# Optimization experiments

Hardware: AMD Instinct MI355X
Metric: run time of the kernel (lower is better)

Reference implementation:

```python
import jax, jax.numpy as jnp
import numpy as np

B, S, D = 4, 2048, 1024  # batch, seq (== context_size), d_in == d_out


def setup_inputs() -> dict:
    key = jax.random.key(0)
    ks = jax.random.split(key, 4)
    scale = 1.0 / np.sqrt(D)
    return {
        "x": jax.random.normal(ks[0], (B, S, D), dtype=jnp.float32),
        "Wq": jax.random.normal(ks[1], (D, D), dtype=jnp.float32) * scale,
        "bq": jnp.zeros((D,), dtype=jnp.float32),
        "Wk": jax.random.normal(ks[2], (D, D), dtype=jnp.float32) * scale,
        "bk": jnp.zeros((D,), dtype=jnp.float32),
        "Wv": jax.random.normal(ks[3], (D, D), dtype=jnp.float32) * scale,
        "bv": jnp.zeros((D,), dtype=jnp.float32),
    }


def reference(x, Wq, bq, Wk, bk, Wv, bv):
    # x: [B, S, D]. Linear layers: y = x @ W^T + b (torch convention: W is [out, in];
    # here W is stored [in, out] already so y = x @ W + b).
    q = jnp.einsum("bsd,df->bsf", x, Wq) + bq
    k = jnp.einsum("bsd,df->bsf", x, Wk) + bk
    v = jnp.einsum("bsd,df->bsf", x, Wv) + bv
    scores = jnp.einsum("bqf,bkf->bqk", q, k)  # [B, S, S]
    causal = jnp.tril(jnp.ones((S, S), dtype=bool))  # mask upper triangle (future)
    scores = jnp.where(causal, scores, -jnp.inf)
    # original divides by sqrt(d_out) after masking
    attn = jax.nn.softmax(scores * (1.0 / jnp.sqrt(jnp.asarray(D, scores.dtype))), axis=-1)
    # dropout rate = 0.0 (identity)
    return jnp.einsum("bqk,bkf->bqf", attn, v)
```

## Files before the change

### kernel.cpp

```cpp
#include <hip/hip_runtime.h>
#include <cstdint>
#include <cstddef>


typedef __attribute__((ext_vector_type(8))) __bf16 bf16x8;
typedef __attribute__((ext_vector_type(4))) float f32x4;
typedef __attribute__((ext_vector_type(4))) float float4v;
typedef __attribute__((ext_vector_type(8))) unsigned short u16x8;
typedef __attribute__((ext_vector_type(4))) unsigned short u16x4;

#define DEVI static __device__ __forceinline__

static constexpr int BB = 4;
static constexpr int SS = 2048;
static constexpr int DD = 1024;
static constexpr float SCALE = 0.03125f;

DEVI unsigned short f2bf(float f) {
  unsigned int u = __builtin_bit_cast(unsigned int, f);
  u += 0x7fffu + ((u >> 16) & 1u);
  return (unsigned short)(u >> 16);
}
DEVI float bf2f(unsigned short h) {
  unsigned int u = ((unsigned int)h) << 16;
  return __builtin_bit_cast(float, u);
}

DEVI void gload16(const void* g, void* l) {
  __builtin_amdgcn_global_load_lds(
      (const __attribute__((address_space(1))) unsigned int*)g,
      (__attribute__((address_space(3))) unsigned int*)l, 16, 0, 0);
}

DEVI void gemm_core(const unsigned short* __restrict__ A,
                    const unsigned short* __restrict__ Bt,
                    int lda, int ldb, int m0, int n0, int K,
                    unsigned short* As, unsigned short* Bs,
                    f32x4 acc[4][4]) {
  const int t = threadIdx.x;
  const int l = t & 63, w = t >> 6;
  const int wr = w >> 1, wc = w & 1;
  const int srow = t >> 2;
  const int scol = (t & 3) * 8;
  const unsigned short* ga0 = A + (size_t)(m0 + srow) * lda + scol;
  const unsigned short* ga1 = ga0 + (size_t)64 * lda;
  const unsigned short* gb0 = Bt + (size_t)(n0 + srow) * ldb + scol;
  const unsigned short* gb1 = gb0 + (size_t)64 * ldb;
  unsigned short* la0 = As + t * 8;
  unsigned short* la1 = As + 2048 + t * 8;
  unsigned short* lb0 = Bs + t * 8;
  unsigned short* lb1 = Bs + 2048 + t * 8;
  const int aoff = (wr * 64 + (l & 15)) * 32 + (l >> 4) * 8;
  const int boff = (wc * 64 + (l & 15)) * 32 + (l >> 4) * 8;
  for (int kk = 0; kk < K; kk += 32) {
    gload16(ga0 + kk, la0);
    gload16(ga1 + kk, la1);
    gload16(gb0 + kk, lb0);
    gload16(gb1 + kk, lb1);
    __syncthreads();
    bf16x8 av[4], bv[4];
#pragma unroll
    for (int i = 0; i < 4; ++i) av[i] = *(const bf16x8*)(As + aoff + i * 512);
#pragma unroll
    for (int i = 0; i < 4; ++i) bv[i] = *(const bf16x8*)(Bs + boff + i * 512);
#pragma unroll
    for (int mi = 0; mi < 4; ++mi)
#pragma unroll
      for (int ni = 0; ni < 4; ++ni)
        acc[mi][ni] = __builtin_amdgcn_mfma_f32_16x16x32_bf16(
            av[mi], bv[ni], acc[mi][ni], 0, 0, 0);
    __syncthreads();
  }
}

__global__ __launch_bounds__(256) void k_conv_x(const float* __restrict__ x,
                                                unsigned short* __restrict__ xb) {
  size_t i = ((size_t)blockIdx.x * 256 + threadIdx.x) * 4;
  float4v v = *(const float4v*)(x + i);
  u16x4 o;
#pragma unroll
  for (int j = 0; j < 4; ++j) o[j] = f2bf(v[j]);
  *(u16x4*)(xb + i) = o;
}

__global__ __launch_bounds__(256) void k_prep_w(const float* __restrict__ Wq,
                                                const float* __restrict__ Wk,
                                                const float* __restrict__ Wv,
                                                unsigned short* __restrict__ Wt) {
  const int z = blockIdx.z;
  const float* W = (z == 0) ? Wq : (z == 1) ? Wk : Wv;
  unsigned short* O = Wt + (size_t)z * DD * DD;
  const int c0 = blockIdx.x * 64, r0 = blockIdx.y * 64;
  __shared__ unsigned short T[64][72];
  const int t = threadIdx.x;
#pragma unroll
  for (int i = 0; i < 4; ++i) {
    int idx = t + i * 256;
    int row = idx >> 4;
    int c4 = (idx & 15) * 4;
    float4v v = *(const float4v*)(W + (size_t)(r0 + row) * DD + c0 + c4);
#pragma unroll
    for (int j = 0; j < 4; ++j) T[row][c4 + j] = f2bf(v[j]);
  }
  __syncthreads();
#pragma unroll
  for (int i = 0; i < 2; ++i) {
    int idx = t + i * 256;
    int n = idx >> 3;
    int g = (idx & 7) * 8;
    u16x8 u;
#pragma unroll
    for (int j = 0; j < 8; ++j) u[j] = T[g + j][n];
    *(u16x8*)(O + (size_t)(c0 + n) * DD + r0 + g) = u;
  }
}

__global__ __launch_bounds__(256) void k_qk_gemm(
    const unsigned short* __restrict__ xb,
    const unsigned short* __restrict__ Wqt,
    const unsigned short* __restrict__ Wkt,
    const float* __restrict__ bq, const float* __restrict__ bk,
    unsigned short* __restrict__ qb, unsigned short* __restrict__ kb) {
  __shared__ unsigned short As[4096], Bs[4096];
  const int z = blockIdx.z;
  const unsigned short* Bt = z ? Wkt : Wqt;
  const float* bias = z ? bk : bq;
  unsigned short* C = z ? kb : qb;
  const int m0 = blockIdx.x * 128, n0 = blockIdx.y * 128;
  f32x4 acc[4][4];
#pragma unroll
  for (int i = 0; i < 4; ++i)
#pragma unroll
    for (int j = 0; j < 4; ++j) acc[i][j] = f32x4{0.f, 0.f, 0.f, 0.f};
  gemm_core(xb, Bt, DD, DD, m0, n0, DD, As, Bs, acc);
  const int t = threadIdx.x, l = t & 63, w = t >> 6, wr = w >> 1, wc = w & 1;
  const int fr = (l >> 4) * 4, fc = l & 15;
#pragma unroll
  for (int mi = 0; mi < 4; ++mi)
#pragma unroll
    for (int ni = 0; ni < 4; ++ni) {
      int gc = n0 + wc * 64 + ni * 16 + fc;
      float bv_ = bias[gc];
#pragma unroll
      for (int r = 0; r < 4; ++r) {
        int gr = m0 + wr * 64 + mi * 16 + fr + r;
        C[(size_t)gr * DD + gc] = f2bf(acc[mi][ni][r] + bv_);
      }
    }
}

__global__ __launch_bounds__(256) void k_vt_gemm(
    const unsigned short* __restrict__ Wvt,
    const unsigned short* __restrict__ xb,
    const float* __restrict__ bv, unsigned short* __restrict__ vt) {
  __shared__ unsigned short As[4096], Bs[4096];
  const int b = blockIdx.z;
  const int m0 = blockIdx.x * 128;
  const int n0 = blockIdx.y * 128;
  f32x4 acc[4][4];
#pragma unroll
  for (int i = 0; i < 4; ++i)
#pragma unroll
    for (int j = 0; j < 4; ++j) acc[i][j] = f32x4{0.f, 0.f, 0.f, 0.f};
  gemm_core(Wvt, xb + (size_t)b * SS * DD, DD, DD, m0, n0, DD, As, Bs, acc);
  unsigned short* C = vt + (size_t)b * DD * SS;
  const int t = threadIdx.x, l = t & 63, w = t >> 6, wr = w >> 1, wc = w & 1;
  const int fr = (l >> 4) * 4, fc = l & 15;
#pragma unroll
  for (int mi = 0; mi < 4; ++mi)
#pragma unroll
    for (int ni = 0; ni < 4; ++ni) {
      int gc = n0 + wc * 64 + ni * 16 + fc;
#pragma unroll
      for (int r = 0; r < 4; ++r) {
        int gr = m0 + wr * 64 + mi * 16 + fr + r;
        C[(size_t)gr * SS + gc] = f2bf(acc[mi][ni][r] + bv[gr]);
      }
    }
}

__global__ __launch_bounds__(256) void k_scores(
    const unsigned short* __restrict__ qb,
    const unsigned short* __restrict__ kb,
    unsigned short* __restrict__ P,
    float* __restrict__ mT, float* __restrict__ lT) {
  const int kt = blockIdx.x, qt = blockIdx.y, b = blockIdx.z;
  if (kt > qt) return;
  __shared__ unsigned short As[4096], Bs[4096];
  __shared__ float redm[2][128];
  __shared__ float redl[2][128];
  f32x4 acc[4][4];
#pragma unroll
  for (int i = 0; i < 4; ++i)
#pragma unroll
    for (int j = 0; j < 4; ++j) acc[i][j] = f32x4{0.f, 0.f, 0.f, 0.f};
  const unsigned short* qp = qb + (size_t)b * SS * DD;
  const unsigned short* kp = kb + (size_t)b * SS * DD;
  gemm_core(qp, kp, DD, DD, qt * 128, kt * 128, DD, As, Bs, acc);

  const int t = threadIdx.x, l = t & 63, w = t >> 6, wr = w >> 1, wc = w & 1;
  const int fr = (l >> 4) * 4, fc = l & 15;
  const bool diag = (kt == qt);
#pragma unroll
  for (int mi = 0; mi < 4; ++mi)
#pragma unroll
    for (int ni = 0; ni < 4; ++ni) {
      int lc = wc * 64 + ni * 16 + fc;
#pragma unroll
      for (int r = 0; r < 4; ++r) {
        int lr = wr * 64 + mi * 16 + fr + r;
        float s = acc[mi][ni][r] * SCALE;
        if (diag && lc > lr) s = -INFINITY;
        acc[mi][ni][r] = s;
      }
    }
  float rmax[4][4];
#pragma unroll
  for (int mi = 0; mi < 4; ++mi)
#pragma unroll
    for (int r = 0; r < 4; ++r) {
      float m = acc[mi][0][r];
#pragma unroll
      for (int ni = 1; ni < 4; ++ni) m = fmaxf(m, acc[mi][ni][r]);
      rmax[mi][r] = m;
    }
#pragma unroll
  for (int d = 1; d < 16; d <<= 1)
#pragma unroll
    for (int mi = 0; mi < 4; ++mi)
#pragma unroll
      for (int r = 0; r < 4; ++r)
        rmax[mi][r] = fmaxf(rmax[mi][r], __shfl_xor(rmax[mi][r], d));
  if ((l & 15) == 0) {
#pragma unroll
    for (int mi = 0; mi < 4; ++mi)
#pragma unroll
      for (int r = 0; r < 4; ++r)
        redm[wc][wr * 64 + mi * 16 + fr + r] = rmax[mi][r];
  }
  __syncthreads();
  float mtv[4][4];
#pragma unroll
  for (int mi = 0; mi < 4; ++mi)
#pragma unroll
    for (int r = 0; r < 4; ++r) {
      int row_l = wr * 64 + mi * 16 + fr + r;
      mtv[mi][r] = fmaxf(redm[0][row_l], redm[1][row_l]);
    }
  float rsum[4][4];
#pragma unroll
  for (int mi = 0; mi < 4; ++mi)
#pragma unroll
    for (int r = 0; r < 4; ++r) rsum[mi][r] = 0.f;
#pragma unroll
  for (int mi = 0; mi < 4; ++mi)
#pragma unroll
    for (int ni = 0; ni < 4; ++ni)
#pragma unroll
      for (int r = 0; r < 4; ++r) {
        float p = __expf(acc[mi][ni][r] - mtv[mi][r]);
        acc[mi][ni][r] = p;
        rsum[mi][r] += p;
      }
#pragma unroll
  for (int d = 1; d < 16; d <<= 1)
#pragma unroll
    for (int mi = 0; mi < 4; ++mi)
#pragma unroll
      for (int r = 0; r < 4; ++r)
        rsum[mi][r] += __shfl_xor(rsum[mi][r], d);
  if ((l & 15) == 0) {
#pragma unroll
    for (int mi = 0; mi < 4; ++mi)
#pragma unroll
      for (int r = 0; r < 4; ++r)
        redl[wc][wr * 64 + mi * 16 + fr + r] = rsum[mi][r];
  }
  __syncthreads();
  if (wc == 0 && (l & 15) == 0) {
#pragma unroll
    for (int mi = 0; mi < 4; ++mi)
#pragma unroll
      for (int r = 0; r < 4; ++r) {
        int row_l = wr * 64 + mi * 16 + fr + r;
        int gq = qt * 128 + row_l;
        mT[((size_t)b * 16 + kt) * SS + gq] = mtv[mi][r];
        lT[((size_t)b * 16 + kt) * SS + gq] = redl[0][row_l] + redl[1][row_l];
      }
  }
  unsigned short* Pp = P + (size_t)b * SS * SS;
#pragma unroll
  for (int mi = 0; mi < 4; ++mi)
#pragma unroll
    for (int ni = 0; ni < 4; ++ni) {
      int gc = kt * 128 + wc * 64 + ni * 16 + fc;
#pragma unroll
      for (int r = 0; r < 4; ++r) {
        int gr = qt * 128 + wr * 64 + mi * 16 + fr + r;
        Pp[(size_t)gr * SS + gc] = f2bf(acc[mi][ni][r]);
      }
    }
}

__global__ __launch_bounds__(256) void k_combine(float* __restrict__ mT,
                                                 const float* __restrict__ lT) {
  const int idx = blockIdx.x * 256 + threadIdx.x;
  const int b = idx >> 11, q = idx & 2047;
  const int qt = q >> 7;
  float mv[16];
  float m = -INFINITY;
#pragma unroll
  for (int kt = 0; kt < 16; ++kt)
    if (kt <= qt) {
      mv[kt] = mT[((size_t)b * 16 + kt) * SS + q];
      m = fmaxf(m, mv[kt]);
    }
  float lsum = 0.f;
#pragma unroll
  for (int kt = 0; kt < 16; ++kt)
    if (kt <= qt) lsum += lT[((size_t)b * 16 + kt) * SS + q] * __expf(mv[kt] - m);
  const float inv = 1.f / lsum;
#pragma unroll
  for (int kt = 0; kt < 16; ++kt)
    if (kt <= qt) mT[((size_t)b * 16 + kt) * SS + q] = __expf(mv[kt] - m) * inv;
}

__global__ __launch_bounds__(256) void k_fixup(unsigned short* __restrict__ P,
                                               const float* __restrict__ F) {
  const int q = blockIdx.x, b = blockIdx.y, t = threadIdx.x;
  const int qt = q >> 7, kt = t >> 4;
  if (kt > qt) return;
  const float f = F[((size_t)b * 16 + kt) * SS + q];
  unsigned short* p = P + (size_t)b * SS * SS + (size_t)q * SS + t * 8;
  u16x8 v = *(const u16x8*)p;
#pragma unroll
  for (int j = 0; j < 8; ++j) v[j] = f2bf(bf2f(v[j]) * f);
  *(u16x8*)p = v;
}

__global__ __launch_bounds__(256) void k_pv(const unsigned short* __restrict__ P,
                                            const unsigned short* __restrict__ vt,
                                            float* __restrict__ out) {
  __shared__ unsigned short As[4096], Bs[4096];
  const int b = blockIdx.z;
  const int n0 = blockIdx.x * 128;
  const int qt = blockIdx.y;
  const int m0 = qt * 128;
  const int Kmax = (qt + 1) * 128;
  f32x4 acc[4][4];
#pragma unroll
  for (int i = 0; i < 4; ++i)
#pragma unroll
    for (int j = 0; j < 4; ++j) acc[i][j] = f32x4{0.f, 0.f, 0.f, 0.f};
  gemm_core(P + (size_t)b * SS * SS, vt + (size_t)b * DD * SS, SS, SS,
            m0, n0, Kmax, As, Bs, acc);
  float* O = out + (size_t)b * SS * DD;
  const int t = threadIdx.x, l = t & 63, w = t >> 6, wr = w >> 1, wc = w & 1;
  const int fr = (l >> 4) * 4, fc = l & 15;
#pragma unroll
  for (int mi = 0; mi < 4; ++mi)
#pragma unroll
    for (int ni = 0; ni < 4; ++ni) {
      int gc = n0 + wc * 64 + ni * 16 + fc;
#pragma unroll
      for (int r = 0; r < 4; ++r) {
        int gr = m0 + wr * 64 + mi * 16 + fr + r;
        O[(size_t)gr * DD + gc] = acc[mi][ni][r];
      }
    }
}

extern "C" void kernel_launch(void* const* d_in, const int* in_sizes, int n_in,
                              void* d_out, int out_size, void* d_ws, size_t ws_size,
                              hipStream_t stream) {
  (void)in_sizes; (void)n_in; (void)out_size; (void)ws_size;
  const float* x  = (const float*)d_in[0];
  const float* Wq = (const float*)d_in[1];
  const float* bq = (const float*)d_in[2];
  const float* Wk = (const float*)d_in[3];
  const float* bk = (const float*)d_in[4];
  const float* Wv = (const float*)d_in[5];
  const float* bv = (const float*)d_in[6];
  float* out = (float*)d_out;

  char* w = (char*)d_ws;
  unsigned short* xb  = (unsigned short*)(w + 0);
  unsigned short* Wt  = (unsigned short*)(w + 16777216);
  unsigned short* qb  = (unsigned short*)(w + 23068672);
  unsigned short* kb  = (unsigned short*)(w + 39845888);
  unsigned short* vt  = (unsigned short*)(w + 56623104);
  unsigned short* P   = (unsigned short*)(w + 73400320);
  float*          mT  = (float*)(w + 106954752);
  float*          lT  = (float*)(w + 107479040);
  unsigned short* Wqt = Wt;
  unsigned short* Wkt = Wt + (size_t)DD * DD;
  unsigned short* Wvt = Wt + (size_t)2 * DD * DD;

  k_conv_x<<<dim3(8192), dim3(256), 0, stream>>>(x, xb);
  k_prep_w<<<dim3(16, 16, 3), dim3(256), 0, stream>>>(Wq, Wk, Wv, Wt);
  k_qk_gemm<<<dim3(64, 8, 2), dim3(256), 0, stream>>>(xb, Wqt, Wkt, bq, bk, qb, kb);
  k_vt_gemm<<<dim3(8, 16, 4), dim3(256), 0, stream>>>(Wvt, xb, bv, vt);
  k_scores<<<dim3(16, 16, 4), dim3(256), 0, stream>>>(qb, kb, P, mT, lT);
  k_combine<<<dim3(32), dim3(256), 0, stream>>>(mT, lT);
  k_fixup<<<dim3(2048, 4), dim3(256), 0, stream>>>(P, mT);
  k_pv<<<dim3(8, 16, 4), dim3(256), 0, stream>>>(P, vt, out);
}
```

Measured before the change: 305.4 us.

## Fold softmax rescale into PV GEMM and use 512-thread GEMM blocks

Removes the separate fixup pass that rescaled every P tile in global memory. The PV kernel now accumulates each 128-wide key chunk into a temporary accumulator and scales it by the per-row, per-chunk factor before adding it to the output. All GEMM kernels also switch from 256-thread blocks with 4x4 MFMA tiles per wave to 512-thread blocks with 4x2 tiles per wave, which lowers register use per wave and adds more waves. The cost is extra per-chunk scaling arithmetic in PV and more LDS traffic per MFMA, since each wave now reuses less data.

```diff
diff --git a/kernel.cpp b/kernel.cpp
--- a/kernel.cpp
+++ b/kernel.cpp
@@ -11,7 +11,6 @@
 
 #define DEVI static __device__ __forceinline__
 
-static constexpr int BB = 4;
 static constexpr int SS = 2048;
 static constexpr int DD = 1024;
 static constexpr float SCALE = 0.03125f;
@@ -32,41 +31,35 @@
       (__attribute__((address_space(3))) unsigned int*)l, 16, 0, 0);
 }
 
-DEVI void gemm_core(const unsigned short* __restrict__ A,
-                    const unsigned short* __restrict__ Bt,
-                    int lda, int ldb, int m0, int n0, int K,
-                    unsigned short* As, unsigned short* Bs,
-                    f32x4 acc[4][4]) {
+DEVI void gemm_core512(const unsigned short* __restrict__ A,
+                       const unsigned short* __restrict__ Bt,
+                       int lda, int ldb, int m0, int n0, int K,
+                       unsigned short* As, unsigned short* Bs,
+                       f32x4 acc[4][2]) {
   const int t = threadIdx.x;
   const int l = t & 63, w = t >> 6;
-  const int wr = w >> 1, wc = w & 1;
+  const int wr = w >> 2, wc = w & 3;
   const int srow = t >> 2;
   const int scol = (t & 3) * 8;
-  const unsigned short* ga0 = A + (size_t)(m0 + srow) * lda + scol;
-  const unsigned short* ga1 = ga0 + (size_t)64 * lda;
-  const unsigned short* gb0 = Bt + (size_t)(n0 + srow) * ldb + scol;
-  const unsigned short* gb1 = gb0 + (size_t)64 * ldb;
-  unsigned short* la0 = As + t * 8;
-  unsigned short* la1 = As + 2048 + t * 8;
-  unsigned short* lb0 = Bs + t * 8;
-  unsigned short* lb1 = Bs + 2048 + t * 8;
+  const unsigned short* ga = A + (size_t)(m0 + srow) * lda + scol;
+  const unsigned short* gb = Bt + (size_t)(n0 + srow) * ldb + scol;
+  unsigned short* la = As + t * 8;
+  unsigned short* lb = Bs + t * 8;
   const int aoff = (wr * 64 + (l & 15)) * 32 + (l >> 4) * 8;
-  const int boff = (wc * 64 + (l & 15)) * 32 + (l >> 4) * 8;
+  const int boff = (wc * 32 + (l & 15)) * 32 + (l >> 4) * 8;
   for (int kk = 0; kk < K; kk += 32) {
-    gload16(ga0 + kk, la0);
-    gload16(ga1 + kk, la1);
-    gload16(gb0 + kk, lb0);
-    gload16(gb1 + kk, lb1);
+    gload16(ga + kk, la);
+    gload16(gb + kk, lb);
     __syncthreads();
-    bf16x8 av[4], bv[4];
+    bf16x8 av[4], bv[2];
 #pragma unroll
     for (int i = 0; i < 4; ++i) av[i] = *(const bf16x8*)(As + aoff + i * 512);
 #pragma unroll
-    for (int i = 0; i < 4; ++i) bv[i] = *(const bf16x8*)(Bs + boff + i * 512);
-#pragma unroll
-    for (int mi = 0; mi < 4; ++mi)
-#pragma unroll
-      for (int ni = 0; ni < 4; ++ni)
+    for (int i = 0; i < 2; ++i) bv[i] = *(const bf16x8*)(Bs + boff + i * 512);
+#pragma unroll
+    for (int mi = 0; mi < 4; ++mi)
+#pragma unroll
+      for (int ni = 0; ni < 2; ++ni)
         acc[mi][ni] = __builtin_amdgcn_mfma_f32_16x16x32_bf16(
             av[mi], bv[ni], acc[mi][ni], 0, 0, 0);
     __syncthreads();
@@ -115,7 +108,7 @@
   }
 }
 
-__global__ __launch_bounds__(256) void k_qk_gemm(
+__global__ __launch_bounds__(512, 4) void k_qk_gemm(
     const unsigned short* __restrict__ xb,
     const unsigned short* __restrict__ Wqt,
     const unsigned short* __restrict__ Wkt,
@@ -127,19 +120,19 @@
   const float* bias = z ? bk : bq;
   unsigned short* C = z ? kb : qb;
   const int m0 = blockIdx.x * 128, n0 = blockIdx.y * 128;
-  f32x4 acc[4][4];
+  f32x4 acc[4][2];
 #pragma unroll
   for (int i = 0; i < 4; ++i)
 #pragma unroll
-    for (int j = 0; j < 4; ++j) acc[i][j] = f32x4{0.f, 0.f, 0.f, 0.f};
-  gemm_core(xb, Bt, DD, DD, m0, n0, DD, As, Bs, acc);
-  const int t = threadIdx.x, l = t & 63, w = t >> 6, wr = w >> 1, wc = w & 1;
+    for (int j = 0; j < 2; ++j) acc[i][j] = f32x4{0.f, 0.f, 0.f, 0.f};
+  gemm_core512(xb, Bt, DD, DD, m0, n0, DD, As, Bs, acc);
+  const int t = threadIdx.x, l = t & 63, w = t >> 6, wr = w >> 2, wc = w & 3;
   const int fr = (l >> 4) * 4, fc = l & 15;
 #pragma unroll
   for (int mi = 0; mi < 4; ++mi)
 #pragma unroll
-    for (int ni = 0; ni < 4; ++ni) {
-      int gc = n0 + wc * 64 + ni * 16 + fc;
+    for (int ni = 0; ni < 2; ++ni) {
+      int gc = n0 + wc * 32 + ni * 16 + fc;
       float bv_ = bias[gc];
 #pragma unroll
       for (int r = 0; r < 4; ++r) {
@@ -149,7 +142,7 @@
     }
 }
 
-__global__ __launch_bounds__(256) void k_vt_gemm(
+__global__ __launch_bounds__(512, 4) void k_vt_gemm(
     const unsigned short* __restrict__ Wvt,
     const unsigned short* __restrict__ xb,
     const float* __restrict__ bv, unsigned short* __restrict__ vt) {
@@ -157,20 +150,20 @@
   const int b = blockIdx.z;
   const int m0 = blockIdx.x * 128;
   const int n0 = blockIdx.y * 128;
-  f32x4 acc[4][4];
+  f32x4 acc[4][2];
 #pragma unroll
   for (int i = 0; i < 4; ++i)
 #pragma unroll
-    for (int j = 0; j < 4; ++j) acc[i][j] = f32x4{0.f, 0.f, 0.f, 0.f};
-  gemm_core(Wvt, xb + (size_t)b * SS * DD, DD, DD, m0, n0, DD, As, Bs, acc);
+    for (int j = 0; j < 2; ++j) acc[i][j] = f32x4{0.f, 0.f, 0.f, 0.f};
+  gemm_core512(Wvt, xb + (size_t)b * SS * DD, DD, DD, m0, n0, DD, As, Bs, acc);
   unsigned short* C = vt + (size_t)b * DD * SS;
-  const int t = threadIdx.x, l = t & 63, w = t >> 6, wr = w >> 1, wc = w & 1;
+  const int t = threadIdx.x, l = t & 63, w = t >> 6, wr = w >> 2, wc = w & 3;
   const int fr = (l >> 4) * 4, fc = l & 15;
 #pragma unroll
   for (int mi = 0; mi < 4; ++mi)
 #pragma unroll
-    for (int ni = 0; ni < 4; ++ni) {
-      int gc = n0 + wc * 64 + ni * 16 + fc;
+    for (int ni = 0; ni < 2; ++ni) {
+      int gc = n0 + wc * 32 + ni * 16 + fc;
 #pragma unroll
       for (int r = 0; r < 4; ++r) {
         int gr = m0 + wr * 64 + mi * 16 + fr + r;
@@ -179,7 +172,7 @@
     }
 }
 
-__global__ __launch_bounds__(256) void k_scores(
+__global__ __launch_bounds__(512, 4) void k_scores(
     const unsigned short* __restrict__ qb,
     const unsigned short* __restrict__ kb,
     unsigned short* __restrict__ P,
@@ -187,25 +180,25 @@
   const int kt = blockIdx.x, qt = blockIdx.y, b = blockIdx.z;
   if (kt > qt) return;
   __shared__ unsigned short As[4096], Bs[4096];
-  __shared__ float redm[2][128];
-  __shared__ float redl[2][128];
-  f32x4 acc[4][4];
+  __shared__ float redm[4][128];
+  __shared__ float redl[4][128];
+  f32x4 acc[4][2];
 #pragma unroll
   for (int i = 0; i < 4; ++i)
 #pragma unroll
-    for (int j = 0; j < 4; ++j) acc[i][j] = f32x4{0.f, 0.f, 0.f, 0.f};
+    for (int j = 0; j < 2; ++j) acc[i][j] = f32x4{0.f, 0.f, 0.f, 0.f};
   const unsigned short* qp = qb + (size_t)b * SS * DD;
   const unsigned short* kp = kb + (size_t)b * SS * DD;
-  gemm_core(qp, kp, DD, DD, qt * 128, kt * 128, DD, As, Bs, acc);
-
-  const int t = threadIdx.x, l = t & 63, w = t >> 6, wr = w >> 1, wc = w & 1;
+  gemm_core512(qp, kp, DD, DD, qt * 128, kt * 128, DD, As, Bs, acc);
+
+  const int t = threadIdx.x, l = t & 63, w = t >> 6, wr = w >> 2, wc = w & 3;
   const int fr = (l >> 4) * 4, fc = l & 15;
   const bool diag = (kt == qt);
 #pragma unroll
   for (int mi = 0; mi < 4; ++mi)
 #pragma unroll
-    for (int ni = 0; ni < 4; ++ni) {
-      int lc = wc * 64 + ni * 16 + fc;
+    for (int ni = 0; ni < 2; ++ni) {
+      int lc = wc * 32 + ni * 16 + fc;
 #pragma unroll
       for (int r = 0; r < 4; ++r) {
         int lr = wr * 64 + mi * 16 + fr + r;
@@ -218,12 +211,8 @@
 #pragma unroll
   for (int mi = 0; mi < 4; ++mi)
 #pragma unroll
-    for (int r = 0; r < 4; ++r) {
-      float m = acc[mi][0][r];
-#pragma unroll
-      for (int ni = 1; ni < 4; ++ni) m = fmaxf(m, acc[mi][ni][r]);
-      rmax[mi][r] = m;
-    }
+    for (int r = 0; r < 4; ++r)
+      rmax[mi][r] = fmaxf(acc[mi][0][r], acc[mi][1][r]);
 #pragma unroll
   for (int d = 1; d < 16; d <<= 1)
 #pragma unroll
@@ -245,22 +234,19 @@
 #pragma unroll
     for (int r = 0; r < 4; ++r) {
       int row_l = wr * 64 + mi * 16 + fr + r;
-      mtv[mi][r] = fmaxf(redm[0][row_l], redm[1][row_l]);
+      mtv[mi][r] = fmaxf(fmaxf(redm[0][row_l], redm[1][row_l]),
+                         fmaxf(redm[2][row_l], redm[3][row_l]));
     }
   float rsum[4][4];
 #pragma unroll
   for (int mi = 0; mi < 4; ++mi)
 #pragma unroll
-    for (int r = 0; r < 4; ++r) rsum[mi][r] = 0.f;
-#pragma unroll
-  for (int mi = 0; mi < 4; ++mi)
-#pragma unroll
-    for (int ni = 0; ni < 4; ++ni)
+    for (int ni = 0; ni < 2; ++ni)
 #pragma unroll
       for (int r = 0; r < 4; ++r) {
         float p = __expf(acc[mi][ni][r] - mtv[mi][r]);
         acc[mi][ni][r] = p;
-        rsum[mi][r] += p;
+        if (ni == 0) rsum[mi][r] = p; else rsum[mi][r] += p;
       }
 #pragma unroll
   for (int d = 1; d < 16; d <<= 1)
@@ -285,15 +271,16 @@
         int row_l = wr * 64 + mi * 16 + fr + r;
         int gq = qt * 128 + row_l;
         mT[((size_t)b * 16 + kt) * SS + gq] = mtv[mi][r];
-        lT[((size_t)b * 16 + kt) * SS + gq] = redl[0][row_l] + redl[1][row_l];
+        lT[((size_t)b * 16 + kt) * SS + gq] =
+            redl[0][row_l] + redl[1][row_l] + redl[2][row_l] + redl[3][row_l];
       }
   }
   unsigned short* Pp = P + (size_t)b * SS * SS;
 #pragma unroll
   for (int mi = 0; mi < 4; ++mi)
 #pragma unroll
-    for (int ni = 0; ni < 4; ++ni) {
-      int gc = kt * 128 + wc * 64 + ni * 16 + fc;
+    for (int ni = 0; ni < 2; ++ni) {
+      int gc = kt * 128 + wc * 32 + ni * 16 + fc;
 #pragma unroll
       for (int r = 0; r < 4; ++r) {
         int gr = qt * 128 + wr * 64 + mi * 16 + fr + r;
@@ -325,47 +312,80 @@
     if (kt <= qt) mT[((size_t)b * 16 + kt) * SS + q] = __expf(mv[kt] - m) * inv;
 }
 
-__global__ __launch_bounds__(256) void k_fixup(unsigned short* __restrict__ P,
-                                               const float* __restrict__ F) {
-  const int q = blockIdx.x, b = blockIdx.y, t = threadIdx.x;
-  const int qt = q >> 7, kt = t >> 4;
-  if (kt > qt) return;
-  const float f = F[((size_t)b * 16 + kt) * SS + q];
-  unsigned short* p = P + (size_t)b * SS * SS + (size_t)q * SS + t * 8;
-  u16x8 v = *(const u16x8*)p;
-#pragma unroll
-  for (int j = 0; j < 8; ++j) v[j] = f2bf(bf2f(v[j]) * f);
-  *(u16x8*)p = v;
-}
-
-__global__ __launch_bounds__(256) void k_pv(const unsigned short* __restrict__ P,
-                                            const unsigned short* __restrict__ vt,
-                                            float* __restrict__ out) {
+__global__ __launch_bounds__(512, 4) void k_pv(
+    const unsigned short* __restrict__ P,
+    const unsigned short* __restrict__ vt,
+    const float* __restrict__ F, float* __restrict__ out) {
   __shared__ unsigned short As[4096], Bs[4096];
+  __shared__ float Flds[2048];
   const int b = blockIdx.z;
   const int n0 = blockIdx.x * 128;
   const int qt = blockIdx.y;
   const int m0 = qt * 128;
-  const int Kmax = (qt + 1) * 128;
-  f32x4 acc[4][4];
+  const int nchunk = qt + 1;
+  const int t = threadIdx.x, l = t & 63, w = t >> 6, wr = w >> 2, wc = w & 3;
+  const int fr = (l >> 4) * 4, fc = l & 15;
+  for (int idx = t; idx < nchunk * 128; idx += 512)
+    Flds[idx] = F[((size_t)b * 16 + (idx >> 7)) * SS + m0 + (idx & 127)];
+  f32x4 accO[4][2], accP[4][2];
 #pragma unroll
   for (int i = 0; i < 4; ++i)
 #pragma unroll
-    for (int j = 0; j < 4; ++j) acc[i][j] = f32x4{0.f, 0.f, 0.f, 0.f};
-  gemm_core(P + (size_t)b * SS * SS, vt + (size_t)b * DD * SS, SS, SS,
-            m0, n0, Kmax, As, Bs, acc);
+    for (int j = 0; j < 2; ++j) {
+      accO[i][j] = f32x4{0.f, 0.f, 0.f, 0.f};
+      accP[i][j] = f32x4{0.f, 0.f, 0.f, 0.f};
+    }
+  const unsigned short* Pp = P + (size_t)b * SS * SS;
+  const unsigned short* Vp = vt + (size_t)b * DD * SS;
+  const int srow = t >> 2, scol = (t & 3) * 8;
+  const unsigned short* ga = Pp + (size_t)(m0 + srow) * SS + scol;
+  const unsigned short* gb = Vp + (size_t)(n0 + srow) * SS + scol;
+  unsigned short* la = As + t * 8;
+  unsigned short* lb = Bs + t * 8;
+  const int aoff = (wr * 64 + (l & 15)) * 32 + (l >> 4) * 8;
+  const int boff = (wc * 32 + (l & 15)) * 32 + (l >> 4) * 8;
+  for (int c = 0; c < nchunk; ++c) {
+#pragma unroll
+    for (int s = 0; s < 4; ++s) {
+      const int kk = c * 128 + s * 32;
+      gload16(ga + kk, la);
+      gload16(gb + kk, lb);
+      __syncthreads();
+      bf16x8 av[4], bv[2];
+#pragma unroll
+      for (int i = 0; i < 4; ++i) av[i] = *(const bf16x8*)(As + aoff + i * 512);
+#pragma unroll
+      for (int i = 0; i < 2; ++i) bv[i] = *(const bf16x8*)(Bs + boff + i * 512);
+#pragma unroll
+      for (int mi = 0; mi < 4; ++mi)
+#pragma unroll
+        for (int ni = 0; ni < 2; ++ni)
+          accP[mi][ni] = __builtin_amdgcn_mfma_f32_16x16x32_bf16(
+              av[mi], bv[ni], accP[mi][ni], 0, 0, 0);
+      __syncthreads();
+    }
+#pragma unroll
+    for (int mi = 0; mi < 4; ++mi)
+#pragma unroll
+      for (int r = 0; r < 4; ++r) {
+        const float f = Flds[c * 128 + wr * 64 + mi * 16 + fr + r];
+#pragma unroll
+        for (int ni = 0; ni < 2; ++ni) {
+          accO[mi][ni][r] += f * accP[mi][ni][r];
+          accP[mi][ni][r] = 0.f;
+        }
+      }
+  }
   float* O = out + (size_t)b * SS * DD;
-  const int t = threadIdx.x, l = t & 63, w = t >> 6, wr = w >> 1, wc = w & 1;
-  const int fr = (l >> 4) * 4, fc = l & 15;
-#pragma unroll
-  for (int mi = 0; mi < 4; ++mi)
-#pragma unroll
-    for (int ni = 0; ni < 4; ++ni) {
-      int gc = n0 + wc * 64 + ni * 16 + fc;
+#pragma unroll
+  for (int mi = 0; mi < 4; ++mi)
+#pragma unroll
+    for (int ni = 0; ni < 2; ++ni) {
+      int gc = n0 + wc * 32 + ni * 16 + fc;
 #pragma unroll
       for (int r = 0; r < 4; ++r) {
         int gr = m0 + wr * 64 + mi * 16 + fr + r;
-        O[(size_t)gr * DD + gc] = acc[mi][ni][r];
+        O[(size_t)gr * DD + gc] = accO[mi][ni][r];
       }
     }
 }
@@ -398,10 +418,9 @@
 
   k_conv_x<<<dim3(8192), dim3(256), 0, stream>>>(x, xb);
   k_prep_w<<<dim3(16, 16, 3), dim3(256), 0, stream>>>(Wq, Wk, Wv, Wt);
-  k_qk_gemm<<<dim3(64, 8, 2), dim3(256), 0, stream>>>(xb, Wqt, Wkt, bq, bk, qb, kb);
-  k_vt_gemm<<<dim3(8, 16, 4), dim3(256), 0, stream>>>(Wvt, xb, bv, vt);
-  k_scores<<<dim3(16, 16, 4), dim3(256), 0, stream>>>(qb, kb, P, mT, lT);
+  k_qk_gemm<<<dim3(64, 8, 2), dim3(512), 0, stream>>>(xb, Wqt, Wkt, bq, bk, qb, kb);
+  k_vt_gemm<<<dim3(8, 16, 4), dim3(512), 0, stream>>>(Wvt, xb, bv, vt);
+  k_scores<<<dim3(16, 16, 4), dim3(512), 0, stream>>>(qb, kb, P, mT, lT);
   k_combine<<<dim3(32), dim3(256), 0, stream>>>(mT, lT);
-  k_fixup<<<dim3(2048, 4), dim3(256), 0, stream>>>(P, mT);
-  k_pv<<<dim3(8, 16, 4), dim3(256), 0, stream>>>(P, vt, out);
-}
+  k_pv<<<dim3(8, 16, 4), dim3(512), 0, stream>>>(P, vt, mT, out);
+}
```

New measurement: 295.5 us. 3.3% less time.
